# Performance work log

Measured on AMD Instinct MI355X. Metric: run time of the kernel, lower is better.

Reference implementation:

```python
import jax, jax.numpy as jnp
import numpy as np

D = 128          # lattice edge (Z = Y = X = 128)
S = 8            # state_size
H = 16           # hidden_size
IN = 7 * S       # own state + 6 neighbor states = 56


def setup_inputs() -> dict:
    key = jax.random.key(0)
    k0, k1, k2 = jax.random.split(key, 3)
    N = D * D * D
    states = jax.random.normal(k0, (N, S), dtype=jnp.float32)
    W1 = jax.random.normal(k1, (IN, H), dtype=jnp.float32) * (1.0 / np.sqrt(IN))
    b1 = jnp.zeros((H,), dtype=jnp.float32)
    W2 = jax.random.normal(k2, (H, S), dtype=jnp.float32) * (1.0 / np.sqrt(H))
    b2 = jnp.zeros((S,), dtype=jnp.float32)
    return {"states": states, "W1": W1, "b1": b1, "W2": W2, "b2": b2}


def reference(states, W1, b1, W2, b2):
    # linear index = z*(X*Y) + y*X + x  ->  grid layout (Z, Y, X, S)
    g = states.reshape(D, D, D, S)
    # 6-neighbor gather with periodic boundary (NEIGHBOR_DIRECTIONS order:
    # (-1,0,0),(1,0,0),(0,-1,0),(0,1,0),(0,0,-1),(0,0,1)); x->axis2, y->axis1, z->axis0.
    # roll(+1) along an axis fetches the neighbor in the -1 direction.
    nbrs = [
        jnp.roll(g,  1, axis=2),  # x-1
        jnp.roll(g, -1, axis=2),  # x+1
        jnp.roll(g,  1, axis=1),  # y-1
        jnp.roll(g, -1, axis=1),  # y+1
        jnp.roll(g,  1, axis=0),  # z-1
        jnp.roll(g, -1, axis=0),  # z+1
    ]
    inp = jnp.concatenate([g] + nbrs, axis=-1)          # (Z, Y, X, 56)
    h = jnp.tanh(jnp.einsum('zyxi,ih->zyxh', inp, W1) + b1)
    out = jnp.einsum('zyxh,hs->zyxs', h, W2) + b2        # (Z, Y, X, 8)
    return out.reshape(-1, S)
```

## Files before the change

kernel.cpp:

```cpp
#include <hip/hip_runtime.h>

#define DIM 128
#define SLOT_STRIDE 2096
#define PLANE_STRIDE (6 * SLOT_STRIDE)

typedef __attribute__((ext_vector_type(8))) short bf16x8;
typedef __attribute__((ext_vector_type(4))) float f32x4;
typedef __attribute__((ext_vector_type(4))) unsigned int u32x4;

static __device__ __forceinline__ unsigned short f2bf_rne(float f) {
    union { float f; unsigned int i; } c; c.f = f;
    unsigned int u = c.i;
    return (unsigned short)((u + 0x7fffu + ((u >> 16) & 1u)) >> 16);
}
static __device__ __forceinline__ unsigned int fbits(float f) {
    union { float f; unsigned int i; } c; c.f = f; return c.i;
}
static __device__ __forceinline__ unsigned int pack_bf16_rne(float lo, float hi) {
    unsigned int ul = fbits(lo), uh = fbits(hi);
    unsigned int tl = ul + 0x7fffu + ((ul >> 16) & 1u);
    unsigned int th = uh + 0x7fffu + ((uh >> 16) & 1u);
    return __builtin_amdgcn_perm(th, tl, 0x07060302u);
}

static __device__ __forceinline__ void barrier_lds_only() {
    asm volatile("s_waitcnt lgkmcnt(0)" ::: "memory");
    __builtin_amdgcn_s_barrier();
    __builtin_amdgcn_sched_barrier(0);
}

struct Frags {
    bf16x8 w1h0, w1h1, w2h;
    f32x4 b1v, b2v;
};

static __device__ __forceinline__ void build_frags(
    const float* W1, const float* b1, const float* W2, const float* b2,
    int col, int quad, Frags& F)
{
#pragma unroll
    for (int j = 0; j < 8; ++j) {
        int k0 = quad * 8 + j;
        F.w1h0[j] = (short)f2bf_rne(W1[k0 * 16 + col]);
        int k1 = 32 + quad * 8 + j;
        F.w1h1[j] = (short)f2bf_rne((k1 < 56) ? W1[k1 * 16 + col] : 0.0f);
        float w2 = (j < 4 && col < 8) ? W2[(quad * 4 + j) * 8 + col] : 0.0f;
        F.w2h[j] = (short)f2bf_rne(w2);
    }
#pragma unroll
    for (int r = 0; r < 4; ++r) {
        F.b1v[r] = b1[quad * 4 + r];
        F.b2v[r] = (quad < 2) ? b2[quad * 4 + r] : 0.0f;
    }
}

__global__ __launch_bounds__(64) void setup_kernel(
    const float* __restrict__ W1, const float* __restrict__ b1,
    const float* __restrict__ W2, const float* __restrict__ b2,
    u32x4* __restrict__ ws)
{
    const int lane = threadIdx.x;
    Frags F;
    build_frags(W1, b1, W2, b2, lane & 15, lane >> 4, F);
    union { bf16x8 v; u32x4 u; } c;
    c.v = F.w1h0; ws[0 * 64 + lane] = c.u;
    c.v = F.w1h1; ws[1 * 64 + lane] = c.u;
    c.v = F.w2h;  ws[2 * 64 + lane] = c.u;
    union { f32x4 v; u32x4 u; } b;
    b.v = F.b1v; ws[3 * 64 + lane] = b.u;
    b.v = F.b2v; ws[4 * 64 + lane] = b.u;
}

template<bool USE_WS>
__global__ __launch_bounds__(256, 3) void lattice_kernel(
    const float* __restrict__ states,
    const float* __restrict__ W1, const float* __restrict__ b1,
    const float* __restrict__ W2, const float* __restrict__ b2,
    float* __restrict__ out, const u32x4* __restrict__ ws)
{
    __shared__ __align__(16) unsigned char lds[4 * PLANE_STRIDE];

    const int tid  = threadIdx.x;
    const int lane = tid & 63;
    const int w    = __builtin_amdgcn_readfirstlane(tid >> 6);
    const int col  = lane & 15;
    const int quad = lane >> 4;

    Frags F;
    if (USE_WS) {
        union { u32x4 u; bf16x8 v; } c;
        c.u = ws[0 * 64 + lane]; F.w1h0 = c.v;
        c.u = ws[1 * 64 + lane]; F.w1h1 = c.v;
        c.u = ws[2 * 64 + lane]; F.w2h  = c.v;
        union { u32x4 u; f32x4 v; } b;
        b.u = ws[3 * 64 + lane]; F.b1v = b.v;
        b.u = ws[4 * 64 + lane]; F.b2v = b.v;
    } else {
        build_frags(W1, b1, W2, b2, col, quad, F);
    }

    const int bI   = blockIdx.x;
    const int slab = bI & 7;
    const int inr  = bI >> 3;
    const int z0   = ((slab << 2) + (inr >> 5)) << 2;
    const int y0   = (inr & 31) << 2;

    auto issue_plane = [&](int zp, f32x4* a, f32x4* b) {
#pragma unroll
        for (int i = 0; i < 3; ++i) {
            const int tk   = w * 3 + i;
            const int r    = tk >> 1;
            const int half = tk & 1;
            const int yr   = (y0 - 1 + r) & 127;
            const float* g = states +
                ((size_t)((((unsigned)(zp & 127)) << 14) + (yr << 7) + (half << 6)) << 3);
            a[i] = *(const f32x4*)(g + (lane << 3));
            b[i] = *(const f32x4*)(g + (lane << 3) + 4);
        }
    };
    auto write_plane = [&](int buf, const f32x4* a, const f32x4* b) {
#pragma unroll
        for (int i = 0; i < 3; ++i) {
            const int tk   = w * 3 + i;
            const int r    = tk >> 1;
            const int half = tk & 1;
            u32x4 p;
            p[0] = __builtin_amdgcn_perm(fbits(a[i][1]), fbits(a[i][0]), 0x07060302u);
            p[1] = __builtin_amdgcn_perm(fbits(a[i][3]), fbits(a[i][2]), 0x07060302u);
            p[2] = __builtin_amdgcn_perm(fbits(b[i][1]), fbits(b[i][0]), 0x07060302u);
            p[3] = __builtin_amdgcn_perm(fbits(b[i][3]), fbits(b[i][2]), 0x07060302u);
            unsigned char* base = lds + buf * PLANE_STRIDE + r * SLOT_STRIDE;
            *(u32x4*)(base + ((half * 64 + lane + 1) << 4)) = p;
            if (half == 0 && lane == 0)  *(u32x4*)(base + 2064) = p;
            if (half == 1 && lane == 63) *(u32x4*)(base) = p;
        }
    };

    const int dxA  = (quad == 1) ? -1 : (quad == 2) ? 1 : 0;
    const int rA   = (quad == 3) ? w : w + 1;
    const int rB   = (quad == 0) ? w + 2 : w + 1;
    const int offA = rA * SLOT_STRIDE + ((col + dxA + 1) << 4);
    const int offB = rB * SLOT_STRIDE + ((col + 1) << 4);

    auto compute_step = [&](int zc, int bufZm, int bufZ, int bufZp) {
        const unsigned char* pA = lds + bufZ * PLANE_STRIDE + offA;
        const int bB = (quad == 1) ? bufZm : (quad == 2) ? bufZp : bufZ;
        const unsigned char* pB = lds + bB * PLANE_STRIDE + offB;
        float* pO = out + (size_t)(((zc << 14) + ((y0 + w) << 7) + col) * 8 + quad * 4);

#pragma unroll
        for (int i = 0; i < 8; ++i) {
            bf16x8 s0f = *(const bf16x8*)(pA + (i << 8));
            bf16x8 s1f = *(const bf16x8*)(pB + (i << 8));

            f32x4 acc = F.b1v;
            acc = __builtin_amdgcn_mfma_f32_16x16x32_bf16(F.w1h0, s0f, acc, 0, 0, 0);
            acc = __builtin_amdgcn_mfma_f32_16x16x32_bf16(F.w1h1, s1f, acc, 0, 0, 0);

            float h0t, h1t, h2t, h3t;
            {
                float e;
                e = __expf(2.0f * acc[0]); h0t = 1.0f - 2.0f * __builtin_amdgcn_rcpf(e + 1.0f);
                e = __expf(2.0f * acc[1]); h1t = 1.0f - 2.0f * __builtin_amdgcn_rcpf(e + 1.0f);
                e = __expf(2.0f * acc[2]); h2t = 1.0f - 2.0f * __builtin_amdgcn_rcpf(e + 1.0f);
                e = __expf(2.0f * acc[3]); h3t = 1.0f - 2.0f * __builtin_amdgcn_rcpf(e + 1.0f);
            }
            union { bf16x8 v; unsigned int u[4]; } hf;
            hf.u[0] = pack_bf16_rne(h0t, h1t);
            hf.u[1] = pack_bf16_rne(h2t, h3t);
            hf.u[2] = 0u;
            hf.u[3] = 0u;

            f32x4 acc2 = F.b2v;
            acc2 = __builtin_amdgcn_mfma_f32_16x16x32_bf16(F.w2h, hf.v, acc2, 0, 0, 0);

            if (quad < 2) {
                __builtin_nontemporal_store(acc2, (f32x4*)(pO + (i << 7)));
            }
        }
    };

    f32x4 Aa[3], Ab[3], Ba[3], Bb[3];
    issue_plane(z0 - 1, Aa, Ab);
    issue_plane(z0,     Ba, Bb);
    write_plane(0, Aa, Ab);
    issue_plane(z0 + 1, Aa, Ab);
    write_plane(1, Ba, Bb);
    issue_plane(z0 + 2, Ba, Bb);
    write_plane(2, Aa, Ab);
    barrier_lds_only();

    issue_plane(z0 + 3, Aa, Ab);
    write_plane(3, Ba, Bb);
    compute_step(z0 + 0, 0, 1, 2);
    barrier_lds_only();
    issue_plane(z0 + 4, Ba, Bb);
    write_plane(0, Aa, Ab);
    compute_step(z0 + 1, 1, 2, 3);
    barrier_lds_only();
    write_plane(1, Ba, Bb);
    compute_step(z0 + 2, 2, 3, 0);
    barrier_lds_only();
    compute_step(z0 + 3, 3, 0, 1);
}

extern "C" void kernel_launch(void* const* d_in, const int* in_sizes, int n_in,
                              void* d_out, int out_size, void* d_ws, size_t ws_size,
                              hipStream_t stream) {
    const float* states = (const float*)d_in[0];
    const float* W1     = (const float*)d_in[1];
    const float* b1     = (const float*)d_in[2];
    const float* W2     = (const float*)d_in[3];
    const float* b2     = (const float*)d_in[4];
    float* out          = (float*)d_out;

    const bool use_ws = ws_size >= (size_t)(5 * 64 * 16);
    if (use_ws) {
        hipLaunchKernelGGL(setup_kernel, dim3(1), dim3(64), 0, stream,
                           W1, b1, W2, b2, (u32x4*)d_ws);
        hipLaunchKernelGGL((lattice_kernel<true>), dim3(1024), dim3(256), 0, stream,
                           states, W1, b1, W2, b2, out, (const u32x4*)d_ws);
    } else {
        hipLaunchKernelGGL((lattice_kernel<false>), dim3(1024), dim3(256), 0, stream,
                           states, W1, b1, W2, b2, out, (const u32x4*)d_ws);
    }
}
```

Measured before the change: 123.8 us.

## Warp-specialize lattice kernel with producer waves and deeper z slabs

Blocks grow to 384 threads: two producer waves stream z-planes from global memory into the 4-slot LDS ring, and four consumer waves run the MFMA MLP on the buffered planes, kept in step by barriers. Each block now covers 8 z-planes instead of 4 and the grid halves to 512 blocks. This cuts the redundant z-halo plane loads and separates global-load latency from compute. The cost is two waves per block that do no math, more registers in the producer waves, and fewer, larger blocks, which lowers the total wave count and can leave CUs less full.

```diff
diff --git a/kernel.cpp b/kernel.cpp
--- a/kernel.cpp
+++ b/kernel.cpp
@@ -1,6 +1,5 @@
 #include <hip/hip_runtime.h>
 
-#define DIM 128
 #define SLOT_STRIDE 2096
 #define PLANE_STRIDE (6 * SLOT_STRIDE)
 
@@ -72,7 +71,7 @@
 }
 
 template<bool USE_WS>
-__global__ __launch_bounds__(256, 3) void lattice_kernel(
+__global__ __launch_bounds__(384, 3) void lattice_kernel(
     const float* __restrict__ states,
     const float* __restrict__ W1, const float* __restrict__ b1,
     const float* __restrict__ W2, const float* __restrict__ b2,
@@ -86,122 +85,132 @@
     const int col  = lane & 15;
     const int quad = lane >> 4;
 
-    Frags F;
-    if (USE_WS) {
-        union { u32x4 u; bf16x8 v; } c;
-        c.u = ws[0 * 64 + lane]; F.w1h0 = c.v;
-        c.u = ws[1 * 64 + lane]; F.w1h1 = c.v;
-        c.u = ws[2 * 64 + lane]; F.w2h  = c.v;
-        union { u32x4 u; f32x4 v; } b;
-        b.u = ws[3 * 64 + lane]; F.b1v = b.v;
-        b.u = ws[4 * 64 + lane]; F.b2v = b.v;
-    } else {
-        build_frags(W1, b1, W2, b2, col, quad, F);
-    }
-
     const int bI   = blockIdx.x;
     const int slab = bI & 7;
     const int inr  = bI >> 3;
-    const int z0   = ((slab << 2) + (inr >> 5)) << 2;
+    const int z0   = slab * 16 + ((inr >> 5) << 3);
     const int y0   = (inr & 31) << 2;
 
-    auto issue_plane = [&](int zp, f32x4* a, f32x4* b) {
-#pragma unroll
-        for (int i = 0; i < 3; ++i) {
-            const int tk   = w * 3 + i;
-            const int r    = tk >> 1;
-            const int half = tk & 1;
-            const int yr   = (y0 - 1 + r) & 127;
-            const float* g = states +
-                ((size_t)((((unsigned)(zp & 127)) << 14) + (yr << 7) + (half << 6)) << 3);
-            a[i] = *(const f32x4*)(g + (lane << 3));
-            b[i] = *(const f32x4*)(g + (lane << 3) + 4);
+    if (w >= 4) {
+        const int wp = w - 4;
+
+        f32x4 Pa[6], Pb[6], Qa[6], Qb[6];
+
+        auto issueP = [&](int zp, f32x4* a, f32x4* b) {
+#pragma unroll
+            for (int i = 0; i < 6; ++i) {
+                const int tk   = wp * 6 + i;
+                const int r    = tk >> 1;
+                const int half = tk & 1;
+                const int yr   = (y0 - 1 + r) & 127;
+                const float* g = states +
+                    ((size_t)((((unsigned)(zp & 127)) << 14) + (yr << 7) + (half << 6)) << 3);
+                a[i] = *(const f32x4*)(g + (lane << 3));
+                b[i] = *(const f32x4*)(g + (lane << 3) + 4);
+            }
+        };
+        auto writeP = [&](int buf, const f32x4* a, const f32x4* b) {
+#pragma unroll
+            for (int i = 0; i < 6; ++i) {
+                const int tk   = wp * 6 + i;
+                const int r    = tk >> 1;
+                const int half = tk & 1;
+                u32x4 p;
+                p[0] = __builtin_amdgcn_perm(fbits(a[i][1]), fbits(a[i][0]), 0x07060302u);
+                p[1] = __builtin_amdgcn_perm(fbits(a[i][3]), fbits(a[i][2]), 0x07060302u);
+                p[2] = __builtin_amdgcn_perm(fbits(b[i][1]), fbits(b[i][0]), 0x07060302u);
+                p[3] = __builtin_amdgcn_perm(fbits(b[i][3]), fbits(b[i][2]), 0x07060302u);
+                unsigned char* base = lds + buf * PLANE_STRIDE + r * SLOT_STRIDE;
+                *(u32x4*)(base + ((half * 64 + lane + 1) << 4)) = p;
+                if (half == 0 && lane == 0)  *(u32x4*)(base + 2064) = p;
+                if (half == 1 && lane == 63) *(u32x4*)(base) = p;
+            }
+        };
+
+        issueP(z0 - 1, Pa, Pb);
+        issueP(z0,     Qa, Qb);
+        writeP(0, Pa, Pb);
+        issueP(z0 + 1, Pa, Pb);
+        writeP(1, Qa, Qb);
+        issueP(z0 + 2, Qa, Qb);
+        writeP(2, Pa, Pb);
+        barrier_lds_only();
+
+        writeP(3, Qa, Qb); issueP(z0 + 3, Qa, Qb); barrier_lds_only();
+        writeP(0, Qa, Qb); issueP(z0 + 4, Qa, Qb); barrier_lds_only();
+        writeP(1, Qa, Qb); issueP(z0 + 5, Qa, Qb); barrier_lds_only();
+        writeP(2, Qa, Qb); issueP(z0 + 6, Qa, Qb); barrier_lds_only();
+        writeP(3, Qa, Qb); issueP(z0 + 7, Qa, Qb); barrier_lds_only();
+        writeP(0, Qa, Qb); issueP(z0 + 8, Qa, Qb); barrier_lds_only();
+        writeP(1, Qa, Qb);                         barrier_lds_only();
+    } else {
+        Frags F;
+        if (USE_WS) {
+            union { u32x4 u; bf16x8 v; } c;
+            c.u = ws[0 * 64 + lane]; F.w1h0 = c.v;
+            c.u = ws[1 * 64 + lane]; F.w1h1 = c.v;
+            c.u = ws[2 * 64 + lane]; F.w2h  = c.v;
+            union { u32x4 u; f32x4 v; } b;
+            b.u = ws[3 * 64 + lane]; F.b1v = b.v;
+            b.u = ws[4 * 64 + lane]; F.b2v = b.v;
+        } else {
+            build_frags(W1, b1, W2, b2, col, quad, F);
         }
-    };
-    auto write_plane = [&](int buf, const f32x4* a, const f32x4* b) {
-#pragma unroll
-        for (int i = 0; i < 3; ++i) {
-            const int tk   = w * 3 + i;
-            const int r    = tk >> 1;
-            const int half = tk & 1;
-            u32x4 p;
-            p[0] = __builtin_amdgcn_perm(fbits(a[i][1]), fbits(a[i][0]), 0x07060302u);
-            p[1] = __builtin_amdgcn_perm(fbits(a[i][3]), fbits(a[i][2]), 0x07060302u);
-            p[2] = __builtin_amdgcn_perm(fbits(b[i][1]), fbits(b[i][0]), 0x07060302u);
-            p[3] = __builtin_amdgcn_perm(fbits(b[i][3]), fbits(b[i][2]), 0x07060302u);
-            unsigned char* base = lds + buf * PLANE_STRIDE + r * SLOT_STRIDE;
-            *(u32x4*)(base + ((half * 64 + lane + 1) << 4)) = p;
-            if (half == 0 && lane == 0)  *(u32x4*)(base + 2064) = p;
-            if (half == 1 && lane == 63) *(u32x4*)(base) = p;
-        }
-    };
-
-    const int dxA  = (quad == 1) ? -1 : (quad == 2) ? 1 : 0;
-    const int rA   = (quad == 3) ? w : w + 1;
-    const int rB   = (quad == 0) ? w + 2 : w + 1;
-    const int offA = rA * SLOT_STRIDE + ((col + dxA + 1) << 4);
-    const int offB = rB * SLOT_STRIDE + ((col + 1) << 4);
-
-    auto compute_step = [&](int zc, int bufZm, int bufZ, int bufZp) {
-        const unsigned char* pA = lds + bufZ * PLANE_STRIDE + offA;
-        const int bB = (quad == 1) ? bufZm : (quad == 2) ? bufZp : bufZ;
-        const unsigned char* pB = lds + bB * PLANE_STRIDE + offB;
-        float* pO = out + (size_t)(((zc << 14) + ((y0 + w) << 7) + col) * 8 + quad * 4);
-
-#pragma unroll
-        for (int i = 0; i < 8; ++i) {
-            bf16x8 s0f = *(const bf16x8*)(pA + (i << 8));
-            bf16x8 s1f = *(const bf16x8*)(pB + (i << 8));
-
-            f32x4 acc = F.b1v;
-            acc = __builtin_amdgcn_mfma_f32_16x16x32_bf16(F.w1h0, s0f, acc, 0, 0, 0);
-            acc = __builtin_amdgcn_mfma_f32_16x16x32_bf16(F.w1h1, s1f, acc, 0, 0, 0);
-
-            float h0t, h1t, h2t, h3t;
-            {
-                float e;
-                e = __expf(2.0f * acc[0]); h0t = 1.0f - 2.0f * __builtin_amdgcn_rcpf(e + 1.0f);
-                e = __expf(2.0f * acc[1]); h1t = 1.0f - 2.0f * __builtin_amdgcn_rcpf(e + 1.0f);
-                e = __expf(2.0f * acc[2]); h2t = 1.0f - 2.0f * __builtin_amdgcn_rcpf(e + 1.0f);
-                e = __expf(2.0f * acc[3]); h3t = 1.0f - 2.0f * __builtin_amdgcn_rcpf(e + 1.0f);
+
+        const int dxA  = (quad == 1) ? -1 : (quad == 2) ? 1 : 0;
+        const int rA   = (quad == 3) ? w : w + 1;
+        const int rB   = (quad == 0) ? w + 2 : w + 1;
+        const int offA = rA * SLOT_STRIDE + ((col + dxA + 1) << 4);
+        const int offB = rB * SLOT_STRIDE + ((col + 1) << 4);
+
+        auto compute_step = [&](int zc, int bufZm, int bufZ, int bufZp) {
+            const unsigned char* pA = lds + bufZ * PLANE_STRIDE + offA;
+            const int bB = (quad == 1) ? bufZm : (quad == 2) ? bufZp : bufZ;
+            const unsigned char* pB = lds + bB * PLANE_STRIDE + offB;
+            float* pO = out + (size_t)(((zc << 14) + ((y0 + w) << 7) + col) * 8 + quad * 4);
+
+#pragma unroll
+            for (int i = 0; i < 8; ++i) {
+                bf16x8 s0f = *(const bf16x8*)(pA + (i << 8));
+                bf16x8 s1f = *(const bf16x8*)(pB + (i << 8));
+
+                f32x4 acc = F.b1v;
+                acc = __builtin_amdgcn_mfma_f32_16x16x32_bf16(F.w1h0, s0f, acc, 0, 0, 0);
+                acc = __builtin_amdgcn_mfma_f32_16x16x32_bf16(F.w1h1, s1f, acc, 0, 0, 0);
+
+                float h0t, h1t, h2t, h3t;
+                {
+                    float e;
+                    e = __expf(2.0f * acc[0]); h0t = 1.0f - 2.0f * __builtin_amdgcn_rcpf(e + 1.0f);
+                    e = __expf(2.0f * acc[1]); h1t = 1.0f - 2.0f * __builtin_amdgcn_rcpf(e + 1.0f);
+                    e = __expf(2.0f * acc[2]); h2t = 1.0f - 2.0f * __builtin_amdgcn_rcpf(e + 1.0f);
+                    e = __expf(2.0f * acc[3]); h3t = 1.0f - 2.0f * __builtin_amdgcn_rcpf(e + 1.0f);
+                }
+                union { bf16x8 v; unsigned int u[4]; } hf;
+                hf.u[0] = pack_bf16_rne(h0t, h1t);
+                hf.u[1] = pack_bf16_rne(h2t, h3t);
+                hf.u[2] = 0u;
+                hf.u[3] = 0u;
+
+                f32x4 acc2 = F.b2v;
+                acc2 = __builtin_amdgcn_mfma_f32_16x16x32_bf16(F.w2h, hf.v, acc2, 0, 0, 0);
+
+                if (quad < 2) {
+                    __builtin_nontemporal_store(acc2, (f32x4*)(pO + (i << 7)));
+                }
             }
-            union { bf16x8 v; unsigned int u[4]; } hf;
-            hf.u[0] = pack_bf16_rne(h0t, h1t);
-            hf.u[1] = pack_bf16_rne(h2t, h3t);
-            hf.u[2] = 0u;
-            hf.u[3] = 0u;
-
-            f32x4 acc2 = F.b2v;
-            acc2 = __builtin_amdgcn_mfma_f32_16x16x32_bf16(F.w2h, hf.v, acc2, 0, 0, 0);
-
-            if (quad < 2) {
-                __builtin_nontemporal_store(acc2, (f32x4*)(pO + (i << 7)));
-            }
-        }
-    };
-
-    f32x4 Aa[3], Ab[3], Ba[3], Bb[3];
-    issue_plane(z0 - 1, Aa, Ab);
-    issue_plane(z0,     Ba, Bb);
-    write_plane(0, Aa, Ab);
-    issue_plane(z0 + 1, Aa, Ab);
-    write_plane(1, Ba, Bb);
-    issue_plane(z0 + 2, Ba, Bb);
-    write_plane(2, Aa, Ab);
-    barrier_lds_only();
-
-    issue_plane(z0 + 3, Aa, Ab);
-    write_plane(3, Ba, Bb);
-    compute_step(z0 + 0, 0, 1, 2);
-    barrier_lds_only();
-    issue_plane(z0 + 4, Ba, Bb);
-    write_plane(0, Aa, Ab);
-    compute_step(z0 + 1, 1, 2, 3);
-    barrier_lds_only();
-    write_plane(1, Ba, Bb);
-    compute_step(z0 + 2, 2, 3, 0);
-    barrier_lds_only();
-    compute_step(z0 + 3, 3, 0, 1);
+        };
+
+        barrier_lds_only();
+        compute_step(z0 + 0, 0, 1, 2); barrier_lds_only();
+        compute_step(z0 + 1, 1, 2, 3); barrier_lds_only();
+        compute_step(z0 + 2, 2, 3, 0); barrier_lds_only();
+        compute_step(z0 + 3, 3, 0, 1); barrier_lds_only();
+        compute_step(z0 + 4, 0, 1, 2); barrier_lds_only();
+        compute_step(z0 + 5, 1, 2, 3); barrier_lds_only();
+        compute_step(z0 + 6, 2, 3, 0); barrier_lds_only();
+        compute_step(z0 + 7, 3, 0, 1);
+    }
 }
 
 extern "C" void kernel_launch(void* const* d_in, const int* in_sizes, int n_in,
@@ -218,10 +227,10 @@
     if (use_ws) {
         hipLaunchKernelGGL(setup_kernel, dim3(1), dim3(64), 0, stream,
                            W1, b1, W2, b2, (u32x4*)d_ws);
-        hipLaunchKernelGGL((lattice_kernel<true>), dim3(1024), dim3(256), 0, stream,
+        hipLaunchKernelGGL((lattice_kernel<true>), dim3(512), dim3(384), 0, stream,
                            states, W1, b1, W2, b2, out, (const u32x4*)d_ws);
     } else {
-        hipLaunchKernelGGL((lattice_kernel<false>), dim3(1024), dim3(256), 0, stream,
+        hipLaunchKernelGGL((lattice_kernel<false>), dim3(512), dim3(384), 0, stream,
                            states, W1, b1, W2, b2, out, (const u32x4*)d_ws);
     }
 }
```

After: 124.6 us. About the same (+0.7%).
